# Optimization experiments

Hardware: AMD Instinct MI355X
Metric: run time of the kernel (lower is better)

Reference implementation:

```python
import jax, jax.numpy as jnp
import numpy as np

E, N, D_IN, D_EMB, H = 4096, 4096, 256, 64, 8
HD = D_EMB * H
N_ETYPES, N_NTYPES = 4, 2
SCALE = D_EMB ** 0.5
EPS = 1e-5


def _layernorm(x, g, b):
    mu = jnp.mean(x, axis=-1, keepdims=True)
    var = jnp.var(x, axis=-1, keepdims=True)
    return (x - mu) / jnp.sqrt(var + EPS) * g + b


def setup_inputs() -> dict:
    key = jax.random.key(0)
    ks = jax.random.split(key, 14)
    s_in = 1.0 / np.sqrt(D_IN)
    s_cat = 1.0 / np.sqrt(HD + D_IN)
    return {
        "hyperedge_features": jax.random.normal(ks[0], (E, D_IN), jnp.float32),
        "node_features": jax.random.normal(ks[1], (N, D_IN), jnp.float32),
        "incidence_matrix": jax.random.randint(ks[2], (N, E), 0, 2, jnp.int32),
        "node_types": jax.random.randint(ks[3], (N,), 0, N_NTYPES, jnp.int32),
        "hyperedge_types": jax.random.randint(ks[4], (E,), 0, N_ETYPES, jnp.int32),
        # per-type expert weights (no bias in torch Linears)
        "Wq": jax.random.uniform(ks[5], (N_ETYPES, D_IN, HD), jnp.float32, -s_in, s_in),
        "Wk": jax.random.uniform(ks[6], (N_NTYPES, D_IN, HD), jnp.float32, -s_in, s_in),
        "Wv": jax.random.uniform(ks[7], (N_NTYPES, D_IN, HD), jnp.float32, -s_in, s_in),
        "Wo": jax.random.uniform(ks[8], (HD + D_IN, D_IN), jnp.float32, -s_cat, s_cat),
        "bo": jax.random.uniform(ks[9], (D_IN,), jnp.float32, -s_cat, s_cat),
        "gamma_e": jnp.ones((D_IN,), jnp.float32),
        "beta_e": jnp.zeros((D_IN,), jnp.float32),
        "gamma_n": jnp.ones((D_IN,), jnp.float32),
        "beta_n": jnp.zeros((D_IN,), jnp.float32),
    }


def reference(hyperedge_features, node_features, incidence_matrix, node_types,
              hyperedge_types, Wq, Wk, Wv, Wo, bo, gamma_e, beta_e, gamma_n, beta_n):
    he = _layernorm(hyperedge_features, gamma_e, beta_e)   # [E, D_IN]
    nf = _layernorm(node_features, gamma_n, beta_n)        # [N, D_IN]

    # type-conditional projections: compute all experts, gather per row
    q = jnp.einsum('ed,tdk->tek', he, Wq)[hyperedge_types, jnp.arange(E)]  # [E, HD]
    k = jnp.einsum('nd,tdk->tnk', nf, Wk)[node_types, jnp.arange(N)]      # [N, HD]
    v = jnp.einsum('nd,tdk->tnk', nf, Wv)[node_types, jnp.arange(N)]      # [N, HD]

    q = q.reshape(E, H, D_EMB).transpose(1, 0, 2)  # [H, E, D]
    k = k.reshape(N, H, D_EMB).transpose(1, 0, 2)  # [H, N, D]
    v = v.reshape(N, H, D_EMB).transpose(1, 0, 2)  # [H, N, D]

    scores = jnp.einsum('hed,hnd->hen', q, k) / SCALE        # [H, E, N]
    mask = incidence_matrix.T[None]                           # [1, E, N]
    scores = jnp.where(mask == 0, -jnp.inf, scores)
    weights = jax.nn.softmax(scores, axis=-1)                 # dropout in eval mode => identity

    out = jnp.einsum('hen,hnd->hed', weights, v)              # [H, E, D]
    out = out.transpose(1, 0, 2).reshape(E, HD)               # [E, HD]
    out = jax.nn.silu(out)

    final = jnp.concatenate([he, out], axis=-1) @ Wo + bo     # [E, D_IN]
    return final, scores
```

## Files before the change

### kernel.cpp

```cpp
#include <hip/hip_runtime.h>
#include <math.h>

#define E 4096
#define NN 4096
#define DIN 256
#define DEMB 64
#define NH 8
#define HD 512
#define EPS 1e-5f

typedef __bf16 bf16x8 __attribute__((ext_vector_type(8)));
typedef float f32x4 __attribute__((ext_vector_type(4)));

union FR { uint4 u; bf16x8 b; };

#define MFMA __builtin_amdgcn_mfma_f32_16x16x32_bf16

__device__ __forceinline__ unsigned pack_hi(float a, float b) {
    return (__float_as_uint(a) >> 16) | (__float_as_uint(b) & 0xffff0000u);
}
__device__ __forceinline__ float residf(float x) {
    return x - __uint_as_float(__float_as_uint(x) & 0xffff0000u);
}

__global__ void zero_counts(int* counts) {
    if (threadIdx.x < 8) counts[threadIdx.x] = 0;
}

__global__ void bucket_kernel(const int* __restrict__ et, const int* __restrict__ nt,
                              int* counts, int* ie, int* in_) {
    int i = blockIdx.x * 256 + threadIdx.x;
    if (i < E) {
        int t = et[i];
        int p = atomicAdd(&counts[t], 1);
        ie[t * E + p] = i;
    } else {
        int j = i - E;
        int t = nt[j];
        int p = atomicAdd(&counts[4 + t], 1);
        in_[t * NN + p] = j;
    }
}

__global__ __launch_bounds__(256) void incbits_kernel(const int* __restrict__ inc,
                                                      unsigned long long* __restrict__ ib) {
    int n = blockIdx.x;
    int l = threadIdx.x & 63, w = threadIdx.x >> 6;
    const int* row = inc + (size_t)n * E;
#pragma unroll
    for (int i = 0; i < 16; i++) {
        int word = i * 4 + w;
        unsigned long long b = __ballot(row[word * 64 + l] != 0);
        if (l == 0) ib[(size_t)n * 64 + word] = b;
    }
}

__device__ __forceinline__ float block_reduce_sum(float v, float* sm) {
    __syncthreads();
#pragma unroll
    for (int o = 32; o > 0; o >>= 1) v += __shfl_down(v, o, 64);
    int w = threadIdx.x >> 6, lane = threadIdx.x & 63;
    if (lane == 0) sm[w] = v;
    __syncthreads();
    return sm[0] + sm[1] + sm[2] + sm[3];
}

__global__ __launch_bounds__(256) void ln_kernel(const float* __restrict__ ef, const float* __restrict__ nf_in,
                          const float* __restrict__ ge, const float* __restrict__ be,
                          const float* __restrict__ gn, const float* __restrict__ bn,
                          float* __restrict__ he, float* __restrict__ nfo) {
    int row = blockIdx.x;
    const float* src; float* dst; const float* g; const float* b;
    if (row < E) { src = ef + (size_t)row * DIN; dst = he + (size_t)row * DIN; g = ge; b = be; }
    else { int r = row - E; src = nf_in + (size_t)r * DIN; dst = nfo + (size_t)r * DIN; g = gn; b = bn; }
    __shared__ float sm[4];
    int t = threadIdx.x;
    float x = src[t];
    float mu = block_reduce_sum(x, sm) * (1.f / DIN);
    float d = x - mu;
    float var = block_reduce_sum(d * d, sm) * (1.f / DIN);
    float rstd = rsqrtf(var + EPS);
    dst[t] = d * rstd * g[t] + b[t];
}

__global__ __launch_bounds__(256) void proj_kernel(const float* __restrict__ X, const float* __restrict__ W,
                            const int* __restrict__ idx, const int* __restrict__ counts,
                            int idxStride, float* __restrict__ out) {
    int t = blockIdx.z;
    int cnt = counts[t];
    int r0 = blockIdx.y * 64;
    if (r0 >= cnt) return;
    int c0 = blockIdx.x * 64;
    const float* Wt = W + (size_t)t * DIN * HD;
    const int* ib = idx + (size_t)t * idxStride;
    __shared__ __align__(16) float Xs[32][68];
    __shared__ __align__(16) float Ws[32][68];
    int tid = threadIdx.x;
    int tr = tid >> 4, tc = tid & 15;
    int lkl = tid & 31, lrb = tid >> 5;
    int wc = tid & 63, wkb = tid >> 6;
    int rIdx[8]; bool rV[8];
#pragma unroll
    for (int i = 0; i < 8; i++) {
        int rl = i * 8 + lrb; int rg = r0 + rl;
        bool vv = rg < cnt; rV[i] = vv;
        rIdx[i] = vv ? ib[rg] : 0;
    }
    float acc[4][4] = {};
    for (int kk = 0; kk < DIN; kk += 32) {
        __syncthreads();
#pragma unroll
        for (int i = 0; i < 8; i++) {
            int rl = i * 8 + lrb;
            Xs[lkl][rl] = rV[i] ? X[(size_t)rIdx[i] * DIN + kk + lkl] : 0.f;
        }
#pragma unroll
        for (int i = 0; i < 8; i++) {
            int kl = i * 4 + wkb;
            Ws[kl][wc] = Wt[(size_t)(kk + kl) * HD + c0 + wc];
        }
        __syncthreads();
#pragma unroll
        for (int kq = 0; kq < 32; kq++) {
            float4 x4 = *(const float4*)&Xs[kq][tr * 4];
            float4 w4 = *(const float4*)&Ws[kq][tc * 4];
            float xa[4] = {x4.x, x4.y, x4.z, x4.w};
            float wa[4] = {w4.x, w4.y, w4.z, w4.w};
#pragma unroll
            for (int i = 0; i < 4; i++)
#pragma unroll
                for (int j = 0; j < 4; j++) acc[i][j] += xa[i] * wa[j];
        }
    }
#pragma unroll
    for (int i = 0; i < 4; i++) {
        int rg = r0 + tr * 4 + i;
        if (rg < cnt) {
            int row = ib[rg];
            *(float4*)&out[(size_t)row * HD + c0 + tc * 4] =
                make_float4(acc[i][0], acc[i][1], acc[i][2], acc[i][3]);
        }
    }
}

__global__ __launch_bounds__(128) void kconv_kernel(const float* __restrict__ kb,
                                                    char* __restrict__ stage) {
    int n = blockIdx.x;
    int t = n >> 6, nl = n & 63;
    int c0 = threadIdx.x * 4;
    int h = c0 >> 6, d = c0 & 63;
    float4 x = *(const float4*)&kb[(size_t)n * HD + c0];
    char* blk = stage + ((size_t)(h * 64 + t) << 15);
    int swz = (nl & 7) << 4;
    float f[4] = {x.x, x.y, x.z, x.w};
#pragma unroll
    for (int i = 0; i < 4; i++) {
        unsigned u = __float_as_uint(f[i]);
        unsigned short hi = (unsigned short)(u >> 16);
        unsigned short lo = (unsigned short)(__float_as_uint(residf(f[i])) >> 16);
        int off = (nl * 128 + (d + i) * 2) ^ swz;
        *(unsigned short*)(blk + off) = hi;
        *(unsigned short*)(blk + 8192 + off) = lo;
    }
}

__global__ __launch_bounds__(256) void vconv_kernel(const float* __restrict__ vb,
                                                    char* __restrict__ stage) {
    int t = blockIdx.x, h = blockIdx.y;
    __shared__ __align__(16) float Ls[64][68];
    int tid = threadIdx.x;
    int n = tid >> 2, q4 = tid & 3;
    const float* src = vb + (size_t)(t * 64 + n) * HD + h * DEMB + q4 * 16;
#pragma unroll
    for (int j = 0; j < 4; j++) {
        float4 x = *(const float4*)(src + j * 4);
        *(float4*)&Ls[n][q4 * 16 + j * 4] = x;
    }
    __syncthreads();
    int d = tid >> 2, nq = (tid & 3) * 16;
    char* blk = stage + ((size_t)(h * 64 + t) << 15);
    int swz = (d & 7) << 4;
#pragma unroll
    for (int i = 0; i < 16; i++) {
        float x = Ls[nq + i][d];
        unsigned u = __float_as_uint(x);
        unsigned short hi = (unsigned short)(u >> 16);
        unsigned short lo = (unsigned short)(__float_as_uint(residf(x)) >> 16);
        int off = (d * 128 + (nq + i) * 2) ^ swz;
        *(unsigned short*)(blk + 16384 + off) = hi;
        *(unsigned short*)(blk + 24576 + off) = lo;
    }
}

__global__ __launch_bounds__(256) void attn_mfma(
    const float* __restrict__ qb, const char* __restrict__ kvstage,
    const unsigned long long* __restrict__ incb,
    float* __restrict__ sc, float* __restrict__ ao)
{
    const int bx = blockIdx.x, h = blockIdx.y;
    const int tid = threadIdx.x;
    const int w = tid >> 6, l = tid & 63;
    const int g = l >> 4, q = l & 15;
    const int e_wave = bx * 128 + w * 32;

    __shared__ __align__(16) char kv[2][32768];
    __shared__ __align__(16) unsigned Pl[4][32 * 68];
    __shared__ unsigned long long Mb[2][64][2];

    FR qh[2][2], ql[2][2];
#pragma unroll
    for (int et = 0; et < 2; et++) {
        const float* qrow = qb + (size_t)(e_wave + et * 16 + q) * HD + h * DEMB;
#pragma unroll
        for (int ks = 0; ks < 2; ks++) {
            const float* p = qrow + ks * 32 + g * 8;
            float4 A = *(const float4*)p;
            float4 B = *(const float4*)(p + 4);
            uint4 uh, ul;
            uh.x = pack_hi(A.x, A.y); uh.y = pack_hi(A.z, A.w);
            uh.z = pack_hi(B.x, B.y); uh.w = pack_hi(B.z, B.w);
            ul.x = pack_hi(residf(A.x), residf(A.y)); ul.y = pack_hi(residf(A.z), residf(A.w));
            ul.z = pack_hi(residf(B.x), residf(B.y)); ul.w = pack_hi(residf(B.z), residf(B.w));
            qh[et][ks].u = uh; ql[et][ks].u = ul;
        }
    }

    uint4 streg[8];
    unsigned long long mreg = 0;
    {
        const char* gs = kvstage + ((size_t)(h * 64) << 15);
#pragma unroll
        for (int i = 0; i < 8; i++) streg[i] = *(const uint4*)(gs + i * 4096 + tid * 16);
        if (tid < 128) mreg = incb[(size_t)(tid >> 1) * 64 + 2 * bx + (tid & 1)];
#pragma unroll
        for (int i = 0; i < 8; i++) *(uint4*)(&kv[0][i * 4096 + tid * 16]) = streg[i];
        if (tid < 128) Mb[0][tid >> 1][tid & 1] = mreg;
    }
    __syncthreads();

    const f32x4 zero4 = {0.f, 0.f, 0.f, 0.f};
    f32x4 oacc[2][4];
#pragma unroll
    for (int et = 0; et < 2; et++)
#pragma unroll
        for (int dt = 0; dt < 4; dt++) oacc[et][dt] = zero4;
    float mrow[2][4], lrow[2][4];
#pragma unroll
    for (int et = 0; et < 2; et++)
#pragma unroll
        for (int r = 0; r < 4; r++) { mrow[et][r] = -INFINITY; lrow[et][r] = 0.f; }

    const int wsel = w >> 1;
    const int shbase = 32 * (w & 1) + 4 * g;

    for (int t = 0; t < 64; t++) {
        const int cur = t & 1, nxt = cur ^ 1;
        if (t < 63) {
            const char* gs = kvstage + ((size_t)(h * 64 + t + 1) << 15);
#pragma unroll
            for (int i = 0; i < 8; i++) streg[i] = *(const uint4*)(gs + i * 4096 + tid * 16);
            if (tid < 128)
                mreg = incb[((size_t)((t + 1) * 64) + (tid >> 1)) * 64 + 2 * bx + (tid & 1)];
        }
        f32x4 sacc[2][4];
#pragma unroll
        for (int et = 0; et < 2; et++)
#pragma unroll
            for (int nt = 0; nt < 4; nt++) sacc[et][nt] = zero4;
        const char* Kh = &kv[cur][0];
        const char* Kl = &kv[cur][8192];
#pragma unroll
        for (int ks = 0; ks < 2; ks++) {
#pragma unroll
            for (int nt = 0; nt < 4; nt++) {
                int nl = nt * 16 + q;
                int off = nl * 128 + ((ks * 64 + g * 16) ^ ((nl & 7) << 4));
                FR bh, bl;
                bh.u = *(const uint4*)(Kh + off);
                bl.u = *(const uint4*)(Kl + off);
#pragma unroll
                for (int et = 0; et < 2; et++) {
                    sacc[et][nt] = MFMA(qh[et][ks].b, bh.b, sacc[et][nt], 0, 0, 0);
                    sacc[et][nt] = MFMA(qh[et][ks].b, bl.b, sacc[et][nt], 0, 0, 0);
                    sacc[et][nt] = MFMA(ql[et][ks].b, bh.b, sacc[et][nt], 0, 0, 0);
                }
            }
        }
        unsigned long long mw[4];
#pragma unroll
        for (int nt = 0; nt < 4; nt++) mw[nt] = Mb[cur][nt * 16 + q][wsel];
        float alpha[2][4];
#pragma unroll
        for (int et = 0; et < 2; et++) {
            float rmax[4] = {-INFINITY, -INFINITY, -INFINITY, -INFINITY};
#pragma unroll
            for (int nt = 0; nt < 4; nt++) {
                unsigned nib = (unsigned)(mw[nt] >> (shbase + 16 * et)) & 0xfu;
                f32x4 s4 = sacc[et][nt];
                float* scp = sc + ((size_t)h * E + (e_wave + et * 16 + g * 4)) * NN
                              + (size_t)t * 64 + nt * 16 + q;
#pragma unroll
                for (int r = 0; r < 4; r++) {
                    float v = s4[r] * 0.125f;
                    bool on = (nib >> r) & 1u;
                    __builtin_nontemporal_store(on ? v : -1.0e30f, scp + (size_t)r * NN);
                    s4[r] = on ? v : -INFINITY;
                    rmax[r] = on ? fmaxf(rmax[r], v) : rmax[r];
                }
                sacc[et][nt] = s4;
            }
#pragma unroll
            for (int o = 1; o < 16; o <<= 1)
#pragma unroll
                for (int r = 0; r < 4; r++) rmax[r] = fmaxf(rmax[r], __shfl_xor(rmax[r], o, 64));
            float ls[4];
#pragma unroll
            for (int r = 0; r < 4; r++) {
                float mo = mrow[et][r];
                float mn = fmaxf(mo, rmax[r]);
                float al = (mn == -INFINITY) ? 1.f : __expf(mo - mn);
                alpha[et][r] = al;
                mrow[et][r] = mn;
                float lacc = 0.f;
#pragma unroll
                for (int nt = 0; nt < 4; nt++) {
                    float sv = sacc[et][nt][r];
                    float p = (sv == -INFINITY) ? 0.f : __expf(sv - mn);
                    sacc[et][nt][r] = p;
                    lacc += p;
                }
                ls[r] = lacc;
            }
#pragma unroll
            for (int o = 1; o < 16; o <<= 1)
#pragma unroll
                for (int r = 0; r < 4; r++) ls[r] += __shfl_xor(ls[r], o, 64);
#pragma unroll
            for (int r = 0; r < 4; r++) lrow[et][r] = lrow[et][r] * alpha[et][r] + ls[r];
        }
        unsigned* Pw = &Pl[w][0];
#pragma unroll
        for (int et = 0; et < 2; et++)
#pragma unroll
            for (int nt = 0; nt < 4; nt++) {
                f32x4 p4 = sacc[et][nt];
#pragma unroll
                for (int r = 0; r < 4; r++) {
                    float p = p4[r];
                    unsigned hu = __float_as_uint(p) & 0xffff0000u;
                    unsigned pk = hu | (__float_as_uint(p - __uint_as_float(hu)) >> 16);
                    Pw[(et * 16 + g * 4 + r) * 68 + nt * 16 + q] = pk;
                }
            }
#pragma unroll
        for (int et = 0; et < 2; et++) {
            f32x4 av;
            av[0] = alpha[et][0]; av[1] = alpha[et][1];
            av[2] = alpha[et][2]; av[3] = alpha[et][3];
#pragma unroll
            for (int dt = 0; dt < 4; dt++) oacc[et][dt] *= av;
        }
        const char* Vh = &kv[cur][16384];
        const char* Vl = &kv[cur][24576];
#pragma unroll
        for (int ns = 0; ns < 2; ns++) {
            FR pah[2], pal[2];
#pragma unroll
            for (int et = 0; et < 2; et++) {
                const unsigned* pr = &Pl[w][(et * 16 + q) * 68 + ns * 32 + g * 8];
                uint4 p0 = *(const uint4*)pr;
                uint4 p1 = *(const uint4*)(pr + 4);
                uint4 hi, lo;
                hi.x = (p0.x >> 16) | (p0.y & 0xffff0000u);
                hi.y = (p0.z >> 16) | (p0.w & 0xffff0000u);
                hi.z = (p1.x >> 16) | (p1.y & 0xffff0000u);
                hi.w = (p1.z >> 16) | (p1.w & 0xffff0000u);
                lo.x = (p0.x & 0xffffu) | (p0.y << 16);
                lo.y = (p0.z & 0xffffu) | (p0.w << 16);
                lo.z = (p1.x & 0xffffu) | (p1.y << 16);
                lo.w = (p1.z & 0xffffu) | (p1.w << 16);
                pah[et].u = hi; pal[et].u = lo;
            }
#pragma unroll
            for (int dt = 0; dt < 4; dt++) {
                int dl = dt * 16 + q;
                int off = dl * 128 + ((ns * 64 + g * 16) ^ ((dl & 7) << 4));
                FR vh, vl;
                vh.u = *(const uint4*)(Vh + off);
                vl.u = *(const uint4*)(Vl + off);
#pragma unroll
                for (int et = 0; et < 2; et++) {
                    oacc[et][dt] = MFMA(pah[et].b, vh.b, oacc[et][dt], 0, 0, 0);
                    oacc[et][dt] = MFMA(pah[et].b, vl.b, oacc[et][dt], 0, 0, 0);
                    oacc[et][dt] = MFMA(pal[et].b, vh.b, oacc[et][dt], 0, 0, 0);
                }
            }
        }
        if (t < 63) {
#pragma unroll
            for (int i = 0; i < 8; i++) *(uint4*)(&kv[nxt][i * 4096 + tid * 16]) = streg[i];
            if (tid < 128) Mb[nxt][tid >> 1][tid & 1] = mreg;
        }
        __syncthreads();
    }
#pragma unroll
    for (int et = 0; et < 2; et++)
#pragma unroll
        for (int r = 0; r < 4; r++) {
            float linv = 1.f / lrow[et][r];
            float* dst = ao + (size_t)(e_wave + et * 16 + g * 4 + r) * HD + h * DEMB;
#pragma unroll
            for (int dt = 0; dt < 4; dt++) dst[dt * 16 + q] = oacc[et][dt][r] * linv;
        }
}

__global__ __launch_bounds__(256) void final_kernel(const float* __restrict__ he, const float* __restrict__ ao,
                             const float* __restrict__ Wo, const float* __restrict__ bo,
                             float* __restrict__ out) {
    int r0 = blockIdx.y * 64, c0 = blockIdx.x * 64;
    __shared__ __align__(16) float As[32][68];
    __shared__ __align__(16) float Bs[32][68];
    int tid = threadIdx.x;
    int tr = tid >> 4, tc = tid & 15;
    int lkl = tid & 31, lrb = tid >> 5;
    int wc = tid & 63, wkb = tid >> 6;
    float acc[4][4] = {};
    for (int kk = 0; kk < DIN + HD; kk += 32) {
        __syncthreads();
        int gk = kk + lkl;
#pragma unroll
        for (int i = 0; i < 8; i++) {
            int rg = r0 + i * 8 + lrb;
            float a;
            if (gk < DIN) a = he[(size_t)rg * DIN + gk];
            else {
                float x = ao[(size_t)rg * HD + gk - DIN];
                a = x / (1.f + __expf(-x));
            }
            As[lkl][i * 8 + lrb] = a;
        }
#pragma unroll
        for (int i = 0; i < 8; i++) {
            int kl = i * 4 + wkb;
            Bs[kl][wc] = Wo[(size_t)(kk + kl) * DIN + c0 + wc];
        }
        __syncthreads();
#pragma unroll
        for (int kq = 0; kq < 32; kq++) {
            float4 a4 = *(const float4*)&As[kq][tr * 4];
            float4 b4 = *(const float4*)&Bs[kq][tc * 4];
            float aa[4] = {a4.x, a4.y, a4.z, a4.w};
            float bb[4] = {b4.x, b4.y, b4.z, b4.w};
#pragma unroll
            for (int i = 0; i < 4; i++)
#pragma unroll
                for (int j = 0; j < 4; j++) acc[i][j] += aa[i] * bb[j];
        }
    }
#pragma unroll
    for (int i = 0; i < 4; i++) {
        float4 r = make_float4(acc[i][0] + bo[c0 + tc * 4 + 0],
                               acc[i][1] + bo[c0 + tc * 4 + 1],
                               acc[i][2] + bo[c0 + tc * 4 + 2],
                               acc[i][3] + bo[c0 + tc * 4 + 3]);
        *(float4*)&out[(size_t)(r0 + tr * 4 + i) * DIN + c0 + tc * 4] = r;
    }
}

extern "C" void kernel_launch(void* const* d_in, const int* in_sizes, int n_in,
                              void* d_out, int out_size, void* d_ws, size_t ws_size,
                              hipStream_t stream) {
    const float* ef     = (const float*)d_in[0];
    const float* nfeat  = (const float*)d_in[1];
    const int*   inc    = (const int*)d_in[2];
    const int*   ntypes = (const int*)d_in[3];
    const int*   etypes = (const int*)d_in[4];
    const float* Wq     = (const float*)d_in[5];
    const float* Wk     = (const float*)d_in[6];
    const float* Wv     = (const float*)d_in[7];
    const float* Wo     = (const float*)d_in[8];
    const float* bo     = (const float*)d_in[9];
    const float* ge     = (const float*)d_in[10];
    const float* be     = (const float*)d_in[11];
    const float* gn     = (const float*)d_in[12];
    const float* bn     = (const float*)d_in[13];

    float* out = (float*)d_out;
    float* sc  = out + (size_t)E * DIN;

    float* ws  = (float*)d_ws;
    float* he  = ws;
    float* nfo = ws + 1048576;
    float* qb  = ws + 2097152;
    float* kb  = ws + 4194304;
    float* vb  = ws + 6291456;
    float* ao  = ws + 8388608;
    int* counts = (int*)(ws + 10485760);
    int* idx_e  = counts + 8;
    int* idx_n  = idx_e + 4 * E;
    char* kvstage = (char*)(ws + 10507264);
    unsigned long long* incb = (unsigned long long*)(ws + 14701568);

    zero_counts<<<1, 64, 0, stream>>>(counts);
    bucket_kernel<<<(E + NN) / 256, 256, 0, stream>>>(etypes, ntypes, counts, idx_e, idx_n);
    incbits_kernel<<<NN, 256, 0, stream>>>(inc, incb);
    ln_kernel<<<E + NN, 256, 0, stream>>>(ef, nfeat, ge, be, gn, bn, he, nfo);
    proj_kernel<<<dim3(8, 64, 4), 256, 0, stream>>>(he, Wq, idx_e, counts, E, qb);
    proj_kernel<<<dim3(8, 64, 2), 256, 0, stream>>>(nfo, Wk, idx_n, counts + 4, NN, kb);
    proj_kernel<<<dim3(8, 64, 2), 256, 0, stream>>>(nfo, Wv, idx_n, counts + 4, NN, vb);
    kconv_kernel<<<NN, 128, 0, stream>>>(kb, kvstage);
    vconv_kernel<<<dim3(64, 8), 256, 0, stream>>>(vb, kvstage);
    attn_mfma<<<dim3(E / 128, NH), 256, 0, stream>>>(qb, kvstage, incb, sc, ao);
    final_kernel<<<dim3(4, 64), 256, 0, stream>>>(he, ao, Wo, bo, out);
}
```

Before: 1.130 ms.

## Move projections and output GEMM to split-bf16 MFMA and split attention over N

The scalar fp32 projection and output GEMMs become bf16x3 MFMA kernels that use pre-swizzled weight images built by a new wconv kernel. The attention kernel is split into two halves along the node dimension (flash-decoding style), and a combine kernel merges the partial max, sum and output. A bit-transposed incidence mask is added so each row reads its mask word directly, and the K/V conversion kernels are vectorized. This adds several launches and extra partial-result traffic in exchange for more parallelism and matrix-core throughput.

```diff
diff --git a/kernel.cpp b/kernel.cpp
--- a/kernel.cpp
+++ b/kernel.cpp
@@ -12,15 +12,16 @@
 typedef __bf16 bf16x8 __attribute__((ext_vector_type(8)));
 typedef float f32x4 __attribute__((ext_vector_type(4)));
 
-union FR { uint4 u; bf16x8 b; };
+union FRS { uint4 u; bf16x8 b; unsigned short s[8]; };
+union H4  { ushort4 u; unsigned short s[4]; };
 
 #define MFMA __builtin_amdgcn_mfma_f32_16x16x32_bf16
 
-__device__ __forceinline__ unsigned pack_hi(float a, float b) {
-    return (__float_as_uint(a) >> 16) | (__float_as_uint(b) & 0xffff0000u);
-}
-__device__ __forceinline__ float residf(float x) {
-    return x - __uint_as_float(__float_as_uint(x) & 0xffff0000u);
+__device__ __forceinline__ void splitf(float f, unsigned short& hs, unsigned short& ls) {
+    unsigned u = __float_as_uint(f);
+    hs = (unsigned short)(u >> 16);
+    float rem = f - __uint_as_float(u & 0xffff0000u);
+    ls = (unsigned short)(__float_as_uint(rem) >> 16);
 }
 
 __global__ void zero_counts(int* counts) {
@@ -53,6 +54,19 @@
         unsigned long long b = __ballot(row[word * 64 + l] != 0);
         if (l == 0) ib[(size_t)n * 64 + word] = b;
     }
+}
+
+__global__ void bit_transpose(const unsigned long long* __restrict__ ib,
+                              unsigned long long* __restrict__ it) {
+    int nw = blockIdx.x, ew = blockIdx.y;
+    int j = threadIdx.x;
+    unsigned long long wv = ib[(size_t)(nw * 64 + j) * 64 + ew];
+    unsigned long long mine = 0;
+    for (int t2 = 0; t2 < 64; t2++) {
+        unsigned long long b = __ballot((int)((wv >> t2) & 1ull));
+        if (t2 == j) mine = b;
+    }
+    it[(size_t)(ew * 64 + j) * 64 + nw] = mine;
 }
 
 __device__ __forceinline__ float block_reduce_sum(float v, float* sm) {
@@ -83,388 +97,425 @@
     dst[t] = d * rstd * g[t] + b[t];
 }
 
-__global__ __launch_bounds__(256) void proj_kernel(const float* __restrict__ X, const float* __restrict__ W,
-                            const int* __restrict__ idx, const int* __restrict__ counts,
-                            int idxStride, float* __restrict__ out) {
+__global__ __launch_bounds__(256) void wconv(const float* __restrict__ src,
+        char* __restrict__ dst, int Ktot, int Ctot) {
+    int cb = blockIdx.x, kb = blockIdx.y, z = blockIdx.z;
+    int CB = Ctot >> 6, KB = Ktot >> 6;
+    const float* S = src + (size_t)z * Ktot * Ctot + (size_t)(kb * 64) * Ctot + cb * 64;
+    char* D = dst + (((size_t)((z * CB + cb) * KB + kb)) << 14);
+    __shared__ float Ls[64][68];
+    int tid = threadIdx.x;
+    int k = tid >> 2, cq = (tid & 3) * 16;
+#pragma unroll
+    for (int j = 0; j < 4; j++)
+        *(float4*)&Ls[k][cq + j * 4] = *(const float4*)&S[(size_t)k * Ctot + cq + j * 4];
+    __syncthreads();
+    int c = tid >> 2, kq = (tid & 3) * 16;
+    int sw = (c & 7) << 4;
+#pragma unroll
+    for (int grp = 0; grp < 4; grp++) {
+        int k0 = kq + grp * 4;
+        H4 hi, lo;
+#pragma unroll
+        for (int i = 0; i < 4; i++) splitf(Ls[k0 + i][c], hi.s[i], lo.s[i]);
+        int off = (c * 128 + k0 * 2) ^ sw;
+        *(ushort4*)(D + off) = hi.u;
+        *(ushort4*)(D + 8192 + off) = lo.u;
+    }
+}
+
+__global__ __launch_bounds__(256) void proj_mfma(const float* __restrict__ X,
+        const char* __restrict__ wimg, const int* __restrict__ idx,
+        const int* __restrict__ counts, int idxStride, int matBase,
+        float* __restrict__ out) {
     int t = blockIdx.z;
     int cnt = counts[t];
     int r0 = blockIdx.y * 64;
     if (r0 >= cnt) return;
-    int c0 = blockIdx.x * 64;
-    const float* Wt = W + (size_t)t * DIN * HD;
+    int cb = blockIdx.x;
     const int* ib = idx + (size_t)t * idxStride;
-    __shared__ __align__(16) float Xs[32][68];
-    __shared__ __align__(16) float Ws[32][68];
     int tid = threadIdx.x;
-    int tr = tid >> 4, tc = tid & 15;
-    int lkl = tid & 31, lrb = tid >> 5;
-    int wc = tid & 63, wkb = tid >> 6;
-    int rIdx[8]; bool rV[8];
-#pragma unroll
-    for (int i = 0; i < 8; i++) {
-        int rl = i * 8 + lrb; int rg = r0 + rl;
-        bool vv = rg < cnt; rV[i] = vv;
-        rIdx[i] = vv ? ib[rg] : 0;
-    }
-    float acc[4][4] = {};
-    for (int kk = 0; kk < DIN; kk += 32) {
+    int w = tid >> 6, l = tid & 63, g = l >> 4, q = l & 15;
+    __shared__ __align__(16) char XW[32768];
+    int sm = tid >> 2, skq = (tid & 3) * 16;
+    int srow = (r0 + sm < cnt) ? ib[r0 + sm] : -1;
+    const int swz = (q & 7) << 4;
+    const int sswz = (sm & 7) << 4;
+    f32x4 acc[4] = {};
+    const char* wtb = wimg + (((size_t)((matBase + t) * 8 + cb) * 4) << 14);
+    for (int kb = 0; kb < 4; kb++) {
         __syncthreads();
 #pragma unroll
-        for (int i = 0; i < 8; i++) {
-            int rl = i * 8 + lrb;
-            Xs[lkl][rl] = rV[i] ? X[(size_t)rIdx[i] * DIN + kk + lkl] : 0.f;
-        }
-#pragma unroll
-        for (int i = 0; i < 8; i++) {
-            int kl = i * 4 + wkb;
-            Ws[kl][wc] = Wt[(size_t)(kk + kl) * HD + c0 + wc];
-        }
+        for (int c4 = 0; c4 < 4; c4++) {
+            int gk = kb * 64 + skq + c4 * 4;
+            float4 xv = (srow >= 0) ? *(const float4*)&X[(size_t)srow * DIN + gk]
+                                    : make_float4(0.f, 0.f, 0.f, 0.f);
+            float xf[4] = {xv.x, xv.y, xv.z, xv.w};
+            H4 hi, lo;
+#pragma unroll
+            for (int i = 0; i < 4; i++) splitf(xf[i], hi.s[i], lo.s[i]);
+            int off = (sm * 128 + (skq + c4 * 4) * 2) ^ sswz;
+            *(ushort4*)(XW + off) = hi.u;
+            *(ushort4*)(XW + 8192 + off) = lo.u;
+        }
+        const char* wt = wtb + ((size_t)kb << 14);
+#pragma unroll
+        for (int i = 0; i < 4; i++)
+            *(uint4*)(XW + 16384 + i * 4096 + tid * 16) = *(const uint4*)(wt + i * 4096 + tid * 16);
         __syncthreads();
-#pragma unroll
-        for (int kq = 0; kq < 32; kq++) {
-            float4 x4 = *(const float4*)&Xs[kq][tr * 4];
-            float4 w4 = *(const float4*)&Ws[kq][tc * 4];
-            float xa[4] = {x4.x, x4.y, x4.z, x4.w};
-            float wa[4] = {w4.x, w4.y, w4.z, w4.w};
-#pragma unroll
-            for (int i = 0; i < 4; i++)
-#pragma unroll
-                for (int j = 0; j < 4; j++) acc[i][j] += xa[i] * wa[j];
-        }
-    }
-#pragma unroll
-    for (int i = 0; i < 4; i++) {
-        int rg = r0 + tr * 4 + i;
-        if (rg < cnt) {
-            int row = ib[rg];
-            *(float4*)&out[(size_t)row * HD + c0 + tc * 4] =
-                make_float4(acc[i][0], acc[i][1], acc[i][2], acc[i][3]);
-        }
-    }
-}
-
-__global__ __launch_bounds__(128) void kconv_kernel(const float* __restrict__ kb,
-                                                    char* __restrict__ stage) {
-    int n = blockIdx.x;
-    int t = n >> 6, nl = n & 63;
-    int c0 = threadIdx.x * 4;
-    int h = c0 >> 6, d = c0 & 63;
-    float4 x = *(const float4*)&kb[(size_t)n * HD + c0];
-    char* blk = stage + ((size_t)(h * 64 + t) << 15);
-    int swz = (nl & 7) << 4;
-    float f[4] = {x.x, x.y, x.z, x.w};
-#pragma unroll
-    for (int i = 0; i < 4; i++) {
-        unsigned u = __float_as_uint(f[i]);
-        unsigned short hi = (unsigned short)(u >> 16);
-        unsigned short lo = (unsigned short)(__float_as_uint(residf(f[i])) >> 16);
-        int off = (nl * 128 + (d + i) * 2) ^ swz;
-        *(unsigned short*)(blk + off) = hi;
-        *(unsigned short*)(blk + 8192 + off) = lo;
-    }
-}
-
-__global__ __launch_bounds__(256) void vconv_kernel(const float* __restrict__ vb,
-                                                    char* __restrict__ stage) {
-    int t = blockIdx.x, h = blockIdx.y;
-    __shared__ __align__(16) float Ls[64][68];
+        FRS bh[2], bl[2];
+#pragma unroll
+        for (int ks = 0; ks < 2; ks++) {
+            int boff = (w * 16 + q) * 128 + ((ks * 64 + g * 16) ^ swz);
+            bh[ks].u = *(const uint4*)(XW + 16384 + boff);
+            bl[ks].u = *(const uint4*)(XW + 24576 + boff);
+        }
+#pragma unroll
+        for (int mt = 0; mt < 4; mt++) {
+#pragma unroll
+            for (int ks = 0; ks < 2; ks++) {
+                int aoff = (mt * 16 + q) * 128 + ((ks * 64 + g * 16) ^ swz);
+                FRS ah, al;
+                ah.u = *(const uint4*)(XW + aoff);
+                al.u = *(const uint4*)(XW + 8192 + aoff);
+                acc[mt] = MFMA(ah.b, bh[ks].b, acc[mt], 0, 0, 0);
+                acc[mt] = MFMA(ah.b, bl[ks].b, acc[mt], 0, 0, 0);
+                acc[mt] = MFMA(al.b, bh[ks].b, acc[mt], 0, 0, 0);
+            }
+        }
+    }
+#pragma unroll
+    for (int mt = 0; mt < 4; mt++)
+#pragma unroll
+        for (int r = 0; r < 4; r++) {
+            int rg = r0 + mt * 16 + 4 * g + r;
+            if (rg < cnt)
+                out[(size_t)ib[rg] * HD + cb * 64 + w * 16 + q] = acc[mt][r];
+        }
+}
+
+__global__ __launch_bounds__(256) void kconv(const float* __restrict__ kbuf,
+                                             char* __restrict__ stage) {
+    int gid = blockIdx.x * 256 + threadIdx.x;
+    int d8 = gid & 7, hh = (gid >> 3) & 7;
+    int n = gid >> 6;
+    const float* src = kbuf + (size_t)n * HD + hh * 64 + d8 * 8;
+    float4 a = *(const float4*)src, b = *(const float4*)(src + 4);
+    float fv[8] = {a.x, a.y, a.z, a.w, b.x, b.y, b.z, b.w};
+    FRS hi, lo;
+#pragma unroll
+    for (int j = 0; j < 8; j++) splitf(fv[j], hi.s[j], lo.s[j]);
+    char* blk = stage + ((size_t)(hh * 64 + (n >> 6)) << 15);
+    int nl = n & 63;
+    int off = (nl * 128 + d8 * 16) ^ ((nl & 7) << 4);
+    *(uint4*)(blk + off) = hi.u;
+    *(uint4*)(blk + 8192 + off) = lo.u;
+}
+
+__global__ __launch_bounds__(256) void vconv(const float* __restrict__ vbuf,
+                                             char* __restrict__ stage) {
+    int tt = blockIdx.x, hh = blockIdx.y;
+    __shared__ float Ls[64][68];
     int tid = threadIdx.x;
-    int n = tid >> 2, q4 = tid & 3;
-    const float* src = vb + (size_t)(t * 64 + n) * HD + h * DEMB + q4 * 16;
-#pragma unroll
-    for (int j = 0; j < 4; j++) {
-        float4 x = *(const float4*)(src + j * 4);
-        *(float4*)&Ls[n][q4 * 16 + j * 4] = x;
-    }
+    int n = tid >> 2, q4 = (tid & 3) * 16;
+#pragma unroll
+    for (int j = 0; j < 4; j++)
+        *(float4*)&Ls[n][q4 + j * 4] =
+            *(const float4*)&vbuf[(size_t)(tt * 64 + n) * HD + hh * DEMB + q4 + j * 4];
     __syncthreads();
-    int d = tid >> 2, nq = (tid & 3) * 16;
-    char* blk = stage + ((size_t)(h * 64 + t) << 15);
-    int swz = (d & 7) << 4;
-#pragma unroll
-    for (int i = 0; i < 16; i++) {
-        float x = Ls[nq + i][d];
-        unsigned u = __float_as_uint(x);
-        unsigned short hi = (unsigned short)(u >> 16);
-        unsigned short lo = (unsigned short)(__float_as_uint(residf(x)) >> 16);
-        int off = (d * 128 + (nq + i) * 2) ^ swz;
-        *(unsigned short*)(blk + 16384 + off) = hi;
-        *(unsigned short*)(blk + 24576 + off) = lo;
-    }
-}
-
-__global__ __launch_bounds__(256) void attn_mfma(
+    char* blk = stage + ((size_t)(hh * 64 + tt) << 15);
+    int d = tid >> 2, ng = tid & 3;
+    int dsw = (d & 7) << 4;
+#pragma unroll
+    for (int sub = 0; sub < 4; sub++) {
+        int n0 = ng * 16 + sub * 4;
+        H4 hi, lo;
+#pragma unroll
+        for (int i = 0; i < 4; i++) splitf(Ls[n0 + i][d], hi.s[i], lo.s[i]);
+        int s0 = ((n0 >> 5) << 5) + (((n0 >> 2) & 3) << 3) + (((n0 >> 4) & 1) << 2);
+        int off = (d * 128 + s0 * 2) ^ dsw;
+        *(ushort4*)(blk + 16384 + off) = hi.u;
+        *(ushort4*)(blk + 24576 + off) = lo.u;
+    }
+}
+
+__global__ __launch_bounds__(256, 2) void attn_mfma(
     const float* __restrict__ qb, const char* __restrict__ kvstage,
-    const unsigned long long* __restrict__ incb,
-    float* __restrict__ sc, float* __restrict__ ao)
+    const unsigned long long* __restrict__ incT,
+    float* __restrict__ sc, float* __restrict__ pO,
+    float* __restrict__ pm, float* __restrict__ plv)
 {
-    const int bx = blockIdx.x, h = blockIdx.y;
+    const int bx = blockIdx.x, h = blockIdx.y, nz = blockIdx.z;
     const int tid = threadIdx.x;
     const int w = tid >> 6, l = tid & 63;
     const int g = l >> 4, q = l & 15;
     const int e_wave = bx * 128 + w * 32;
+    const int T0 = nz * 32;
 
     __shared__ __align__(16) char kv[2][32768];
-    __shared__ __align__(16) unsigned Pl[4][32 * 68];
-    __shared__ unsigned long long Mb[2][64][2];
-
-    FR qh[2][2], ql[2][2];
+
+    FRS qh[2][2], ql[2][2];
 #pragma unroll
     for (int et = 0; et < 2; et++) {
         const float* qrow = qb + (size_t)(e_wave + et * 16 + q) * HD + h * DEMB;
 #pragma unroll
         for (int ks = 0; ks < 2; ks++) {
-            const float* p = qrow + ks * 32 + g * 8;
-            float4 A = *(const float4*)p;
-            float4 B = *(const float4*)(p + 4);
-            uint4 uh, ul;
-            uh.x = pack_hi(A.x, A.y); uh.y = pack_hi(A.z, A.w);
-            uh.z = pack_hi(B.x, B.y); uh.w = pack_hi(B.z, B.w);
-            ul.x = pack_hi(residf(A.x), residf(A.y)); ul.y = pack_hi(residf(A.z), residf(A.w));
-            ul.z = pack_hi(residf(B.x), residf(B.y)); ul.w = pack_hi(residf(B.z), residf(B.w));
-            qh[et][ks].u = uh; ql[et][ks].u = ul;
+            float4 A = *(const float4*)(qrow + ks * 32 + g * 8);
+            float4 B = *(const float4*)(qrow + ks * 32 + g * 8 + 4);
+            float fv[8] = {A.x, A.y, A.z, A.w, B.x, B.y, B.z, B.w};
+            FRS hh, ll;
+#pragma unroll
+            for (int j = 0; j < 8; j++) splitf(fv[j], hh.s[j], ll.s[j]);
+            qh[et][ks] = hh; ql[et][ks] = ll;
         }
     }
 
     uint4 streg[8];
-    unsigned long long mreg = 0;
     {
-        const char* gs = kvstage + ((size_t)(h * 64) << 15);
+        const char* gs = kvstage + ((size_t)(h * 64 + T0) << 15);
 #pragma unroll
         for (int i = 0; i < 8; i++) streg[i] = *(const uint4*)(gs + i * 4096 + tid * 16);
-        if (tid < 128) mreg = incb[(size_t)(tid >> 1) * 64 + 2 * bx + (tid & 1)];
 #pragma unroll
         for (int i = 0; i < 8; i++) *(uint4*)(&kv[0][i * 4096 + tid * 16]) = streg[i];
-        if (tid < 128) Mb[0][tid >> 1][tid & 1] = mreg;
     }
     __syncthreads();
 
-    const f32x4 zero4 = {0.f, 0.f, 0.f, 0.f};
     f32x4 oacc[2][4];
 #pragma unroll
     for (int et = 0; et < 2; et++)
 #pragma unroll
-        for (int dt = 0; dt < 4; dt++) oacc[et][dt] = zero4;
-    float mrow[2][4], lrow[2][4];
-#pragma unroll
-    for (int et = 0; et < 2; et++)
-#pragma unroll
-        for (int r = 0; r < 4; r++) { mrow[et][r] = -INFINITY; lrow[et][r] = 0.f; }
-
-    const int wsel = w >> 1;
-    const int shbase = 32 * (w & 1) + 4 * g;
-
-    for (int t = 0; t < 64; t++) {
-        const int cur = t & 1, nxt = cur ^ 1;
-        if (t < 63) {
+        for (int dt = 0; dt < 4; dt++) oacc[et][dt] = (f32x4){0.f, 0.f, 0.f, 0.f};
+    float mrow[2] = {-INFINITY, -INFINITY}, lrow[2] = {0.f, 0.f};
+    const int swz = (q & 7) << 4;
+
+    for (int tt = 0; tt < 32; tt++) {
+        const int t = T0 + tt;
+        const int cur = tt & 1;
+        if (tt < 31) {
             const char* gs = kvstage + ((size_t)(h * 64 + t + 1) << 15);
 #pragma unroll
             for (int i = 0; i < 8; i++) streg[i] = *(const uint4*)(gs + i * 4096 + tid * 16);
-            if (tid < 128)
-                mreg = incb[((size_t)((t + 1) * 64) + (tid >> 1)) * 64 + 2 * bx + (tid & 1)];
         }
         f32x4 sacc[2][4];
 #pragma unroll
         for (int et = 0; et < 2; et++)
 #pragma unroll
-            for (int nt = 0; nt < 4; nt++) sacc[et][nt] = zero4;
+            for (int nt = 0; nt < 4; nt++) sacc[et][nt] = (f32x4){0.f, 0.f, 0.f, 0.f};
         const char* Kh = &kv[cur][0];
         const char* Kl = &kv[cur][8192];
 #pragma unroll
         for (int ks = 0; ks < 2; ks++) {
 #pragma unroll
             for (int nt = 0; nt < 4; nt++) {
-                int nl = nt * 16 + q;
-                int off = nl * 128 + ((ks * 64 + g * 16) ^ ((nl & 7) << 4));
-                FR bh, bl;
-                bh.u = *(const uint4*)(Kh + off);
-                bl.u = *(const uint4*)(Kl + off);
+                int off = (nt * 16 + q) * 128 + ((ks * 64 + g * 16) ^ swz);
+                FRS ah, al;
+                ah.u = *(const uint4*)(Kh + off);
+                al.u = *(const uint4*)(Kl + off);
 #pragma unroll
                 for (int et = 0; et < 2; et++) {
-                    sacc[et][nt] = MFMA(qh[et][ks].b, bh.b, sacc[et][nt], 0, 0, 0);
-                    sacc[et][nt] = MFMA(qh[et][ks].b, bl.b, sacc[et][nt], 0, 0, 0);
-                    sacc[et][nt] = MFMA(ql[et][ks].b, bh.b, sacc[et][nt], 0, 0, 0);
+                    sacc[et][nt] = MFMA(ah.b, qh[et][ks].b, sacc[et][nt], 0, 0, 0);
+                    sacc[et][nt] = MFMA(ah.b, ql[et][ks].b, sacc[et][nt], 0, 0, 0);
+                    sacc[et][nt] = MFMA(al.b, qh[et][ks].b, sacc[et][nt], 0, 0, 0);
                 }
             }
         }
-        unsigned long long mw[4];
-#pragma unroll
-        for (int nt = 0; nt < 4; nt++) mw[nt] = Mb[cur][nt * 16 + q][wsel];
-        float alpha[2][4];
+        float alpha_s[2];
 #pragma unroll
         for (int et = 0; et < 2; et++) {
-            float rmax[4] = {-INFINITY, -INFINITY, -INFINITY, -INFINITY};
+            int e = e_wave + et * 16 + q;
+            unsigned long long mw = incT[(size_t)e * 64 + t];
+            float rmax = -INFINITY;
 #pragma unroll
             for (int nt = 0; nt < 4; nt++) {
-                unsigned nib = (unsigned)(mw[nt] >> (shbase + 16 * et)) & 0xfu;
+                unsigned nib = (unsigned)(mw >> (nt * 16 + g * 4)) & 0xfu;
                 f32x4 s4 = sacc[et][nt];
-                float* scp = sc + ((size_t)h * E + (e_wave + et * 16 + g * 4)) * NN
-                              + (size_t)t * 64 + nt * 16 + q;
+                f32x4 w4;
 #pragma unroll
                 for (int r = 0; r < 4; r++) {
                     float v = s4[r] * 0.125f;
                     bool on = (nib >> r) & 1u;
-                    __builtin_nontemporal_store(on ? v : -1.0e30f, scp + (size_t)r * NN);
+                    w4[r] = on ? v : -1.0e30f;
                     s4[r] = on ? v : -INFINITY;
-                    rmax[r] = on ? fmaxf(rmax[r], v) : rmax[r];
+                    if (on) rmax = fmaxf(rmax, v);
+                }
+                __builtin_nontemporal_store(w4,
+                    (f32x4*)(sc + ((size_t)h * E + e) * NN + (size_t)t * 64 + nt * 16 + g * 4));
+                sacc[et][nt] = s4;
+            }
+            rmax = fmaxf(rmax, __shfl_xor(rmax, 16, 64));
+            rmax = fmaxf(rmax, __shfl_xor(rmax, 32, 64));
+            float mo = mrow[et];
+            float mn = fmaxf(mo, rmax);
+            float al = (mn == -INFINITY) ? 1.f : __expf(mo - mn);
+            alpha_s[et] = al;
+            mrow[et] = mn;
+            float ls = 0.f;
+#pragma unroll
+            for (int nt = 0; nt < 4; nt++) {
+                f32x4 s4 = sacc[et][nt];
+#pragma unroll
+                for (int r = 0; r < 4; r++) {
+                    float p = (s4[r] == -INFINITY) ? 0.f : __expf(s4[r] - mn);
+                    s4[r] = p; ls += p;
                 }
                 sacc[et][nt] = s4;
             }
-#pragma unroll
-            for (int o = 1; o < 16; o <<= 1)
-#pragma unroll
-                for (int r = 0; r < 4; r++) rmax[r] = fmaxf(rmax[r], __shfl_xor(rmax[r], o, 64));
-            float ls[4];
-#pragma unroll
-            for (int r = 0; r < 4; r++) {
-                float mo = mrow[et][r];
-                float mn = fmaxf(mo, rmax[r]);
-                float al = (mn == -INFINITY) ? 1.f : __expf(mo - mn);
-                alpha[et][r] = al;
-                mrow[et][r] = mn;
-                float lacc = 0.f;
-#pragma unroll
-                for (int nt = 0; nt < 4; nt++) {
-                    float sv = sacc[et][nt][r];
-                    float p = (sv == -INFINITY) ? 0.f : __expf(sv - mn);
-                    sacc[et][nt][r] = p;
-                    lacc += p;
-                }
-                ls[r] = lacc;
-            }
-#pragma unroll
-            for (int o = 1; o < 16; o <<= 1)
-#pragma unroll
-                for (int r = 0; r < 4; r++) ls[r] += __shfl_xor(ls[r], o, 64);
-#pragma unroll
-            for (int r = 0; r < 4; r++) lrow[et][r] = lrow[et][r] * alpha[et][r] + ls[r];
-        }
-        unsigned* Pw = &Pl[w][0];
+            ls += __shfl_xor(ls, 16, 64);
+            ls += __shfl_xor(ls, 32, 64);
+            lrow[et] = lrow[et] * al + ls;
+        }
 #pragma unroll
         for (int et = 0; et < 2; et++)
 #pragma unroll
-            for (int nt = 0; nt < 4; nt++) {
-                f32x4 p4 = sacc[et][nt];
-#pragma unroll
-                for (int r = 0; r < 4; r++) {
-                    float p = p4[r];
-                    unsigned hu = __float_as_uint(p) & 0xffff0000u;
-                    unsigned pk = hu | (__float_as_uint(p - __uint_as_float(hu)) >> 16);
-                    Pw[(et * 16 + g * 4 + r) * 68 + nt * 16 + q] = pk;
-                }
-            }
-#pragma unroll
-        for (int et = 0; et < 2; et++) {
-            f32x4 av;
-            av[0] = alpha[et][0]; av[1] = alpha[et][1];
-            av[2] = alpha[et][2]; av[3] = alpha[et][3];
-#pragma unroll
-            for (int dt = 0; dt < 4; dt++) oacc[et][dt] *= av;
-        }
+            for (int dt = 0; dt < 4; dt++) oacc[et][dt] *= alpha_s[et];
         const char* Vh = &kv[cur][16384];
         const char* Vl = &kv[cur][24576];
 #pragma unroll
         for (int ns = 0; ns < 2; ns++) {
-            FR pah[2], pal[2];
+            FRS pah[2], pal[2];
 #pragma unroll
             for (int et = 0; et < 2; et++) {
-                const unsigned* pr = &Pl[w][(et * 16 + q) * 68 + ns * 32 + g * 8];
-                uint4 p0 = *(const uint4*)pr;
-                uint4 p1 = *(const uint4*)(pr + 4);
-                uint4 hi, lo;
-                hi.x = (p0.x >> 16) | (p0.y & 0xffff0000u);
-                hi.y = (p0.z >> 16) | (p0.w & 0xffff0000u);
-                hi.z = (p1.x >> 16) | (p1.y & 0xffff0000u);
-                hi.w = (p1.z >> 16) | (p1.w & 0xffff0000u);
-                lo.x = (p0.x & 0xffffu) | (p0.y << 16);
-                lo.y = (p0.z & 0xffffu) | (p0.w << 16);
-                lo.z = (p1.x & 0xffffu) | (p1.y << 16);
-                lo.w = (p1.z & 0xffffu) | (p1.w << 16);
-                pah[et].u = hi; pal[et].u = lo;
+                FRS ph, pl2;
+#pragma unroll
+                for (int w2 = 0; w2 < 4; w2++) {
+                    int nt = 2 * ns + (w2 >> 1);
+                    int rb = 2 * (w2 & 1);
+                    splitf(sacc[et][nt][rb],     ph.s[2 * w2],     pl2.s[2 * w2]);
+                    splitf(sacc[et][nt][rb + 1], ph.s[2 * w2 + 1], pl2.s[2 * w2 + 1]);
+                }
+                pah[et] = ph; pal[et] = pl2;
             }
 #pragma unroll
             for (int dt = 0; dt < 4; dt++) {
-                int dl = dt * 16 + q;
-                int off = dl * 128 + ((ns * 64 + g * 16) ^ ((dl & 7) << 4));
-                FR vh, vl;
+                int off = (dt * 16 + q) * 128 + ((ns * 64 + g * 16) ^ swz);
+                FRS vh, vl;
                 vh.u = *(const uint4*)(Vh + off);
                 vl.u = *(const uint4*)(Vl + off);
 #pragma unroll
                 for (int et = 0; et < 2; et++) {
-                    oacc[et][dt] = MFMA(pah[et].b, vh.b, oacc[et][dt], 0, 0, 0);
-                    oacc[et][dt] = MFMA(pah[et].b, vl.b, oacc[et][dt], 0, 0, 0);
-                    oacc[et][dt] = MFMA(pal[et].b, vh.b, oacc[et][dt], 0, 0, 0);
+                    oacc[et][dt] = MFMA(vh.b, pah[et].b, oacc[et][dt], 0, 0, 0);
+                    oacc[et][dt] = MFMA(vh.b, pal[et].b, oacc[et][dt], 0, 0, 0);
+                    oacc[et][dt] = MFMA(vl.b, pah[et].b, oacc[et][dt], 0, 0, 0);
                 }
             }
         }
-        if (t < 63) {
-#pragma unroll
-            for (int i = 0; i < 8; i++) *(uint4*)(&kv[nxt][i * 4096 + tid * 16]) = streg[i];
-            if (tid < 128) Mb[nxt][tid >> 1][tid & 1] = mreg;
+        if (tt < 31) {
+#pragma unroll
+            for (int i = 0; i < 8; i++) *(uint4*)(&kv[cur ^ 1][i * 4096 + tid * 16]) = streg[i];
         }
         __syncthreads();
     }
 #pragma unroll
-    for (int et = 0; et < 2; et++)
+    for (int et = 0; et < 2; et++) {
+        int e = e_wave + et * 16 + q;
+        size_t base = (((size_t)h * E + e) * 2 + nz) * 64;
+#pragma unroll
+        for (int dt = 0; dt < 4; dt++) {
+            *(float4*)&pO[base + dt * 16 + g * 4] =
+                make_float4(oacc[et][dt][0], oacc[et][dt][1], oacc[et][dt][2], oacc[et][dt][3]);
+        }
+        if (g == 0) {
+            pm[((size_t)h * E + e) * 2 + nz] = mrow[et];
+            plv[((size_t)h * E + e) * 2 + nz] = lrow[et];
+        }
+    }
+}
+
+__global__ __launch_bounds__(256) void combine_kernel(const float* __restrict__ pO,
+        const float* __restrict__ pm, const float* __restrict__ plv,
+        float* __restrict__ ao) {
+    int gid = blockIdx.x * 256 + threadIdx.x;
+    int eh = gid >> 2, dq = (gid & 3) * 16;
+    float m0 = pm[(size_t)eh * 2], m1 = pm[(size_t)eh * 2 + 1];
+    float l0 = plv[(size_t)eh * 2], l1 = plv[(size_t)eh * 2 + 1];
+    float m = fmaxf(m0, m1);
+    float w0 = (m0 == -INFINITY) ? 0.f : __expf(m0 - m);
+    float w1 = (m1 == -INFINITY) ? 0.f : __expf(m1 - m);
+    float den = w0 * l0 + w1 * l1;
+    float rinv = den > 0.f ? 1.f / den : 0.f;
+    int h = eh >> 12, e = eh & 4095;
+    const float* o0 = pO + (size_t)eh * 128;
+    const float* o1 = o0 + 64;
+    float* dst = ao + (size_t)e * HD + h * DEMB + dq;
+#pragma unroll
+    for (int j = 0; j < 4; j++) {
+        float4 a = *(const float4*)(o0 + dq + j * 4);
+        float4 b = *(const float4*)(o1 + dq + j * 4);
+        *(float4*)(dst + j * 4) = make_float4(
+            (w0 * a.x + w1 * b.x) * rinv, (w0 * a.y + w1 * b.y) * rinv,
+            (w0 * a.z + w1 * b.z) * rinv, (w0 * a.w + w1 * b.w) * rinv);
+    }
+}
+
+__global__ __launch_bounds__(256) void final_mfma(const float* __restrict__ he,
+        const float* __restrict__ ao, const char* __restrict__ woimg,
+        const float* __restrict__ bo, float* __restrict__ out) {
+    int cb = blockIdx.x, rb = blockIdx.y;
+    int tid = threadIdx.x;
+    int w = tid >> 6, l = tid & 63, g = l >> 4, q = l & 15;
+    __shared__ __align__(16) char XW[32768];
+    int sm = tid >> 2, skq = (tid & 3) * 16;
+    int grow = rb * 64 + sm;
+    const int swz = (q & 7) << 4;
+    const int sswz = (sm & 7) << 4;
+    f32x4 acc[4] = {};
+    for (int kb = 0; kb < 12; kb++) {
+        __syncthreads();
+#pragma unroll
+        for (int c4 = 0; c4 < 4; c4++) {
+            int gk = kb * 64 + skq + c4 * 4;
+            float4 xv;
+            if (gk < DIN) {
+                xv = *(const float4*)&he[(size_t)grow * DIN + gk];
+            } else {
+                xv = *(const float4*)&ao[(size_t)grow * HD + gk - DIN];
+                xv.x = xv.x / (1.f + __expf(-xv.x));
+                xv.y = xv.y / (1.f + __expf(-xv.y));
+                xv.z = xv.z / (1.f + __expf(-xv.z));
+                xv.w = xv.w / (1.f + __expf(-xv.w));
+            }
+            float xf[4] = {xv.x, xv.y, xv.z, xv.w};
+            H4 hi, lo;
+#pragma unroll
+            for (int i = 0; i < 4; i++) splitf(xf[i], hi.s[i], lo.s[i]);
+            int off = (sm * 128 + (skq + c4 * 4) * 2) ^ sswz;
+            *(ushort4*)(XW + off) = hi.u;
+            *(ushort4*)(XW + 8192 + off) = lo.u;
+        }
+        const char* wt = woimg + (((size_t)(cb * 12 + kb)) << 14);
+#pragma unroll
+        for (int i = 0; i < 4; i++)
+            *(uint4*)(XW + 16384 + i * 4096 + tid * 16) = *(const uint4*)(wt + i * 4096 + tid * 16);
+        __syncthreads();
+        FRS bh[2], bl[2];
+#pragma unroll
+        for (int ks = 0; ks < 2; ks++) {
+            int boff = (w * 16 + q) * 128 + ((ks * 64 + g * 16) ^ swz);
+            bh[ks].u = *(const uint4*)(XW + 16384 + boff);
+            bl[ks].u = *(const uint4*)(XW + 24576 + boff);
+        }
+#pragma unroll
+        for (int mt = 0; mt < 4; mt++) {
+#pragma unroll
+            for (int ks = 0; ks < 2; ks++) {
+                int aoff = (mt * 16 + q) * 128 + ((ks * 64 + g * 16) ^ swz);
+                FRS ah, al;
+                ah.u = *(const uint4*)(XW + aoff);
+                al.u = *(const uint4*)(XW + 8192 + aoff);
+                acc[mt] = MFMA(ah.b, bh[ks].b, acc[mt], 0, 0, 0);
+                acc[mt] = MFMA(ah.b, bl[ks].b, acc[mt], 0, 0, 0);
+                acc[mt] = MFMA(al.b, bh[ks].b, acc[mt], 0, 0, 0);
+            }
+        }
+    }
+    float bv = bo[cb * 64 + w * 16 + q];
+#pragma unroll
+    for (int mt = 0; mt < 4; mt++)
 #pragma unroll
         for (int r = 0; r < 4; r++) {
-            float linv = 1.f / lrow[et][r];
-            float* dst = ao + (size_t)(e_wave + et * 16 + g * 4 + r) * HD + h * DEMB;
-#pragma unroll
-            for (int dt = 0; dt < 4; dt++) dst[dt * 16 + q] = oacc[et][dt][r] * linv;
-        }
-}
-
-__global__ __launch_bounds__(256) void final_kernel(const float* __restrict__ he, const float* __restrict__ ao,
-                             const float* __restrict__ Wo, const float* __restrict__ bo,
-                             float* __restrict__ out) {
-    int r0 = blockIdx.y * 64, c0 = blockIdx.x * 64;
-    __shared__ __align__(16) float As[32][68];
-    __shared__ __align__(16) float Bs[32][68];
-    int tid = threadIdx.x;
-    int tr = tid >> 4, tc = tid & 15;
-    int lkl = tid & 31, lrb = tid >> 5;
-    int wc = tid & 63, wkb = tid >> 6;
-    float acc[4][4] = {};
-    for (int kk = 0; kk < DIN + HD; kk += 32) {
-        __syncthreads();
-        int gk = kk + lkl;
-#pragma unroll
-        for (int i = 0; i < 8; i++) {
-            int rg = r0 + i * 8 + lrb;
-            float a;
-            if (gk < DIN) a = he[(size_t)rg * DIN + gk];
-            else {
-                float x = ao[(size_t)rg * HD + gk - DIN];
-                a = x / (1.f + __expf(-x));
-            }
-            As[lkl][i * 8 + lrb] = a;
-        }
-#pragma unroll
-        for (int i = 0; i < 8; i++) {
-            int kl = i * 4 + wkb;
-            Bs[kl][wc] = Wo[(size_t)(kk + kl) * DIN + c0 + wc];
-        }
-        __syncthreads();
-#pragma unroll
-        for (int kq = 0; kq < 32; kq++) {
-            float4 a4 = *(const float4*)&As[kq][tr * 4];
-            float4 b4 = *(const float4*)&Bs[kq][tc * 4];
-            float aa[4] = {a4.x, a4.y, a4.z, a4.w};
-            float bb[4] = {b4.x, b4.y, b4.z, b4.w};
-#pragma unroll
-            for (int i = 0; i < 4; i++)
-#pragma unroll
-                for (int j = 0; j < 4; j++) acc[i][j] += aa[i] * bb[j];
-        }
-    }
-#pragma unroll
-    for (int i = 0; i < 4; i++) {
-        float4 r = make_float4(acc[i][0] + bo[c0 + tc * 4 + 0],
-                               acc[i][1] + bo[c0 + tc * 4 + 1],
-                               acc[i][2] + bo[c0 + tc * 4 + 2],
-                               acc[i][3] + bo[c0 + tc * 4 + 3]);
-        *(float4*)&out[(size_t)(r0 + tr * 4 + i) * DIN + c0 + tc * 4] = r;
-    }
+            out[(size_t)(rb * 64 + mt * 16 + 4 * g + r) * DIN + cb * 64 + w * 16 + q] =
+                acc[mt][r] + bv;
+        }
 }
 
 extern "C" void kernel_launch(void* const* d_in, const int* in_sizes, int n_in,
@@ -498,18 +549,30 @@
     int* counts = (int*)(ws + 10485760);
     int* idx_e  = counts + 8;
     int* idx_n  = idx_e + 4 * E;
-    char* kvstage = (char*)(ws + 10507264);
-    unsigned long long* incb = (unsigned long long*)(ws + 14701568);
+    char* kvstage = (char*)(ws + 10510848);
+    unsigned long long* incb = (unsigned long long*)(ws + 14705152);
+    unsigned long long* incT = (unsigned long long*)(ws + 15229440);
+    char* wimg  = (char*)(ws + 15753728);
+    char* woimg = (char*)(ws + 16802304);
+    float* pO   = kb;
+    float* pm   = ws + 16998912;
+    float* plv  = ws + 17064448;
 
     zero_counts<<<1, 64, 0, stream>>>(counts);
     bucket_kernel<<<(E + NN) / 256, 256, 0, stream>>>(etypes, ntypes, counts, idx_e, idx_n);
     incbits_kernel<<<NN, 256, 0, stream>>>(inc, incb);
+    bit_transpose<<<dim3(64, 64), 64, 0, stream>>>(incb, incT);
     ln_kernel<<<E + NN, 256, 0, stream>>>(ef, nfeat, ge, be, gn, bn, he, nfo);
-    proj_kernel<<<dim3(8, 64, 4), 256, 0, stream>>>(he, Wq, idx_e, counts, E, qb);
-    proj_kernel<<<dim3(8, 64, 2), 256, 0, stream>>>(nfo, Wk, idx_n, counts + 4, NN, kb);
-    proj_kernel<<<dim3(8, 64, 2), 256, 0, stream>>>(nfo, Wv, idx_n, counts + 4, NN, vb);
-    kconv_kernel<<<NN, 128, 0, stream>>>(kb, kvstage);
-    vconv_kernel<<<dim3(64, 8), 256, 0, stream>>>(vb, kvstage);
-    attn_mfma<<<dim3(E / 128, NH), 256, 0, stream>>>(qb, kvstage, incb, sc, ao);
-    final_kernel<<<dim3(4, 64), 256, 0, stream>>>(he, ao, Wo, bo, out);
-}
+    wconv<<<dim3(8, 4, 4), 256, 0, stream>>>(Wq, wimg, DIN, HD);
+    wconv<<<dim3(8, 4, 2), 256, 0, stream>>>(Wk, wimg + (size_t)4 * 524288, DIN, HD);
+    wconv<<<dim3(8, 4, 2), 256, 0, stream>>>(Wv, wimg + (size_t)6 * 524288, DIN, HD);
+    wconv<<<dim3(4, 12, 1), 256, 0, stream>>>(Wo, woimg, DIN + HD, DIN);
+    proj_mfma<<<dim3(8, 64, 4), 256, 0, stream>>>(he, wimg, idx_e, counts, E, 0, qb);
+    proj_mfma<<<dim3(8, 64, 2), 256, 0, stream>>>(nfo, wimg, idx_n, counts + 4, NN, 4, kb);
+    proj_mfma<<<dim3(8, 64, 2), 256, 0, stream>>>(nfo, wimg, idx_n, counts + 4, NN, 6, vb);
+    kconv<<<1024, 256, 0, stream>>>(kb, kvstage);
+    vconv<<<dim3(64, 8), 256, 0, stream>>>(vb, kvstage);
+    attn_mfma<<<dim3(32, 8, 2), 256, 0, stream>>>(qb, kvstage, incT, sc, pO, pm, plv);
+    combine_kernel<<<512, 256, 0, stream>>>(pO, pm, plv, ao);
+    final_mfma<<<dim3(4, 64), 256, 0, stream>>>(he, ao, woimg, bo, out);
+}
```

Result: faster. 948.0 us (-16.1%).
